# Optimization experiments

Measured on AMD Instinct MI355X. Metric: run time of the kernel, lower is better.

The kernel has to match this reference:

```python
import math
import jax, jax.numpy as jnp
import numpy as np

N, D, E, H = 4096, 512, 64, 8
LN_EPS = 1e-5


def setup_inputs() -> dict:
    key = jax.random.key(0)
    ks = jax.random.split(key, 6)
    return {
        "x": jax.random.normal(ks[0], (N, D), jnp.float32),
        "wq": jax.random.normal(ks[1], (H, D, E), jnp.float32) * 0.05,
        "wk": jax.random.normal(ks[2], (H, D, E), jnp.float32) * 0.05,
        "wv": jax.random.normal(ks[3], (H, D, E), jnp.float32) * 0.05,
        "w_mh": jax.random.normal(ks[4], (H * E, D), jnp.float32) * 0.05,
        "ln1_g": jnp.ones((D,), jnp.float32),
        "ln1_b": jnp.zeros((D,), jnp.float32),
        "ffn_w": jax.random.normal(ks[5], (D, D), jnp.float32) * 0.05,  # torch Linear weight [out,in]
        "ffn_b": jnp.zeros((D,), jnp.float32),
        "ln2_g": jnp.ones((D,), jnp.float32),
        "ln2_b": jnp.zeros((D,), jnp.float32),
    }


def _layernorm(y, g, b):
    m = y.mean(-1, keepdims=True)
    v = ((y - m) ** 2).mean(-1, keepdims=True)
    return (y - m) * jax.lax.rsqrt(v + LN_EPS) * g + b


def reference(x, wq, wk, wv, w_mh, ln1_g, ln1_b, ffn_w, ffn_b, ln2_g, ln2_b):
    dk = math.sqrt(wk.shape[-1])  # sqrt(embedding_size), as in the torch code
    q = jnp.einsum('nd,hde->hne', x, wq)  # [H,N,E]
    k = jnp.einsum('nd,hde->hne', x, wk)
    v = jnp.einsum('nd,hde->hne', x, wv)
    scores = jax.nn.softmax(jnp.einsum('hne,hme->hnm', q, k) / dk, axis=-1)  # [H,N,N]
    z = jnp.einsum('hnm,hme->hne', scores, v)  # [H,N,E]
    concat_z = jnp.transpose(z, (1, 0, 2)).reshape(x.shape[0], -1)  # [N, H*E]
    transformed_z = concat_z @ w_mh  # [N, D]
    normed_z = _layernorm(transformed_z + x, ln1_g, ln1_b)
    out = normed_z @ ffn_w.T + ffn_b  # nn.Linear
    return _layernorm(out + normed_z, ln2_g, ln2_b)
```

## Files before the change

kernel.cpp:

```cpp
#include <hip/hip_runtime.h>

#define NN 4096
#define DD 512
#define EE 64
#define HH 8

typedef _Float16 f16;
typedef f16 f16x4 __attribute__((ext_vector_type(4)));
typedef f16 f16x8 __attribute__((ext_vector_type(8)));
typedef float f32x4 __attribute__((ext_vector_type(4)));

__device__ __forceinline__ float hexp2(float x) { return __builtin_amdgcn_exp2f(x); }

__device__ void tile_transpose_cvt(const float* __restrict__ src, f16* __restrict__ dst,
                                   int R, int C, int bx, int by, int tid)
{
    __shared__ float t[32][33];
    const int tx = tid & 31, ty = tid >> 5;
    #pragma unroll
    for (int i = 0; i < 4; ++i) {
        int r = ty + i * 8;
        t[r][tx] = src[(size_t)(by + r) * C + bx + tx];
    }
    __syncthreads();
    #pragma unroll
    for (int i = 0; i < 4; ++i) {
        int c = ty + i * 8;
        dst[(size_t)(bx + c) * R + by + tx] = (f16)t[tx][c];
    }
}

__global__ __launch_bounds__(256) void prep_kernel(
    const float* __restrict__ x, const float* __restrict__ ffn_w,
    const float* __restrict__ wq, const float* __restrict__ wk, const float* __restrict__ wv,
    const float* __restrict__ w_mh,
    f16* __restrict__ xh, f16* __restrict__ ffnT, f16* __restrict__ wqkvT, f16* __restrict__ wmhT)
{
    const int job = blockIdx.y;
    const int tid = threadIdx.x;
    if (job == 0) {
        size_t i = ((size_t)blockIdx.x * 256 + tid) * 4;
        const size_t step = (size_t)256 * 256 * 4;
        for (; i < (size_t)NN * DD; i += step) {
            float4 t = *(const float4*)(x + i);
            f16x4 h = { (f16)t.x, (f16)t.y, (f16)t.z, (f16)t.w };
            *(f16x4*)(xh + i) = h;
        }
    } else if (job == 1) {
        size_t i = ((size_t)blockIdx.x * 256 + tid) * 4;
        float4 t = *(const float4*)(ffn_w + i);
        f16x4 h = { (f16)t.x, (f16)t.y, (f16)t.z, (f16)t.w };
        *(f16x4*)(ffnT + i) = h;
    } else if (job <= 4) {
        const float* src = (job == 2) ? wq : (job == 3) ? wk : wv;
        f16* dst = wqkvT + (size_t)(job - 2) * HH * EE * DD;
        const int z = blockIdx.x >> 5;
        const int tile = blockIdx.x & 31;
        tile_transpose_cvt(src + (size_t)z * DD * EE, dst + (size_t)z * DD * EE,
                           DD, EE, (tile & 1) * 32, (tile >> 1) * 32, tid);
    } else {
        const int tile = blockIdx.x;
        tile_transpose_cvt(w_mh, wmhT, DD, DD, (tile & 15) * 32, (tile >> 4) * 32, tid);
    }
}

__global__ __launch_bounds__(256) void qkv_mfma_kernel(
    const f16* __restrict__ A, const f16* __restrict__ BT,
    f16* __restrict__ qh, f16* __restrict__ kh, f16* __restrict__ vTh)
{
    __shared__ f16 As[64][72];
    __shared__ f16 Bs[64][72];
    const int tid = threadIdx.x;
    const int n0 = blockIdx.x * 64;
    const int cb = blockIdx.y;
    const int sel = cb >> 3, h = cb & 7;
    const f16* Arow = A + (size_t)n0 * DD;
    const f16* Brow = BT + (size_t)cb * 64 * DD;

    const int lane = tid & 63, wave = tid >> 6;
    const int l16 = lane & 15, quad = lane >> 4;
    const int m0 = wave * 16;

    const int r1 = tid >> 3, c1 = (tid & 7) * 8;
    const int r2 = (tid + 256) >> 3, c2 = ((tid + 256) & 7) * 8;

    f32x4 acc[4];
    #pragma unroll
    for (int t = 0; t < 4; ++t) acc[t] = (f32x4){0.f, 0.f, 0.f, 0.f};

    f16x8 a1 = *(const f16x8*)(Arow + (size_t)r1 * DD + c1);
    f16x8 a2 = *(const f16x8*)(Arow + (size_t)r2 * DD + c2);
    f16x8 b1 = *(const f16x8*)(Brow + (size_t)r1 * DD + c1);
    f16x8 b2 = *(const f16x8*)(Brow + (size_t)r2 * DD + c2);

    for (int kt = 0; kt < DD; kt += 64) {
        __syncthreads();
        *(f16x8*)(&As[r1][c1]) = a1;
        *(f16x8*)(&As[r2][c2]) = a2;
        *(f16x8*)(&Bs[r1][c1]) = b1;
        *(f16x8*)(&Bs[r2][c2]) = b2;
        __syncthreads();
        if (kt + 64 < DD) {
            a1 = *(const f16x8*)(Arow + (size_t)r1 * DD + kt + 64 + c1);
            a2 = *(const f16x8*)(Arow + (size_t)r2 * DD + kt + 64 + c2);
            b1 = *(const f16x8*)(Brow + (size_t)r1 * DD + kt + 64 + c1);
            b2 = *(const f16x8*)(Brow + (size_t)r2 * DD + kt + 64 + c2);
        }
        #pragma unroll
        for (int kk = 0; kk < 64; kk += 32) {
            f16x8 a = *(const f16x8*)(&As[m0 + l16][kk + quad * 8]);
            #pragma unroll
            for (int t = 0; t < 4; ++t) {
                f16x8 b = *(const f16x8*)(&Bs[t * 16 + l16][kk + quad * 8]);
                acc[t] = __builtin_amdgcn_mfma_f32_16x16x32_f16(a, b, acc[t], 0, 0, 0);
            }
        }
    }

    if (sel == 2) {
        #pragma unroll
        for (int t = 0; t < 4; ++t) {
            int e = t * 16 + l16;
            f16x4 v = { (f16)acc[t][0], (f16)acc[t][1], (f16)acc[t][2], (f16)acc[t][3] };
            *(f16x4*)(vTh + ((size_t)h * EE + e) * NN + n0 + m0 + quad * 4) = v;
        }
    } else {
        f16* o = (sel == 0) ? qh : kh;
        const float s = (sel == 0) ? 0.125f * 1.44269504088896f : 1.0f;
        #pragma unroll
        for (int r = 0; r < 4; ++r) {
            int row = n0 + m0 + quad * 4 + r;
            #pragma unroll
            for (int t = 0; t < 4; ++t)
                o[(size_t)h * NN * EE + (size_t)row * EE + t * 16 + l16] = (f16)(acc[t][r] * s);
        }
    }
}

#define BQ 128
#define BK 64
#define LK (BK + 12)

__global__ __launch_bounds__(256) void attn_mfma_kernel(
    const f16* __restrict__ q, const f16* __restrict__ k,
    const f16* __restrict__ vT, f16* __restrict__ Opart, float* __restrict__ lpart)
{
    __shared__ f16 Ks[BK][LK];
    __shared__ f16 VsT[EE][LK];

    const int tid = threadIdx.x;
    const int h = blockIdx.y;
    const int n0 = blockIdx.x * BQ;
    const int sp = blockIdx.z;
    const int nsp = gridDim.z;
    const int wave = tid >> 6;
    const int lane = tid & 63;
    const int l16 = lane & 15;
    const int quad = lane >> 4;
    const int m0 = wave * 16;

    const f16* qh = q + (size_t)h * NN * EE;
    const f16* kh = k + (size_t)h * NN * EE;
    const f16* vh = vT + (size_t)h * NN * EE;

    f16x8 qf[2][2];
    #pragma unroll
    for (int s = 0; s < 2; ++s) {
        const f16* qb = qh + (size_t)(n0 + s * 64 + m0 + l16) * EE;
        qf[s][0] = *(const f16x8*)(qb + quad * 8);
        qf[s][1] = *(const f16x8*)(qb + 32 + quad * 8);
    }

    float lp[2] = {0.f, 0.f};
    f32x4 O[2][4];
    #pragma unroll
    for (int s = 0; s < 2; ++s)
        #pragma unroll
        for (int t = 0; t < 4; ++t) O[s][t] = (f32x4){0.f, 0.f, 0.f, 0.f};

    const int span = NN / nsp;
    const int k_begin = sp * span;
    const int k_end = k_begin + span;

    const int srow = tid >> 3, sc8 = (tid & 7) * 8;
    const int srow2 = (tid + 256) >> 3, sc82 = ((tid + 256) & 7) * 8;
    #define KPERM(kk_) (((kk_) & 0x23) | (((kk_) & 0x04) << 2) | (((kk_) & 0x18) >> 1))
    const int prow1 = KPERM(srow), prow2 = KPERM(srow2);

    f16x8 kr0 = *(const f16x8*)(kh + (size_t)(k_begin + srow) * EE + sc8);
    f16x8 kr1 = *(const f16x8*)(kh + (size_t)(k_begin + srow2) * EE + sc82);
    f16x8 vr0 = *(const f16x8*)(vh + (size_t)srow * NN + k_begin + sc8);
    f16x8 vr1 = *(const f16x8*)(vh + (size_t)srow2 * NN + k_begin + sc82);

    for (int kt = k_begin; kt < k_end; kt += BK) {
        __syncthreads();
        *(f16x8*)(&Ks[prow1][sc8]) = kr0;
        *(f16x8*)(&Ks[prow2][sc82]) = kr1;
        *(f16x8*)(&VsT[srow][sc8]) = vr0;
        *(f16x8*)(&VsT[srow2][sc82]) = vr1;
        __syncthreads();

        if (kt + BK < k_end) {
            kr0 = *(const f16x8*)(kh + (size_t)(kt + BK + srow) * EE + sc8);
            kr1 = *(const f16x8*)(kh + (size_t)(kt + BK + srow2) * EE + sc82);
            vr0 = *(const f16x8*)(vh + (size_t)srow * NN + kt + BK + sc8);
            vr1 = *(const f16x8*)(vh + (size_t)srow2 * NN + kt + BK + sc82);
        }

        f16x8 bf[2][2];
        #pragma unroll
        for (int t = 0; t < 4; ++t) {
            f16x8 a0 = *(const f16x8*)(&Ks[t * 16 + l16][quad * 8]);
            f16x8 a1 = *(const f16x8*)(&Ks[t * 16 + l16][32 + quad * 8]);
            #pragma unroll
            for (int s = 0; s < 2; ++s) {
                f32x4 st = {0.f, 0.f, 0.f, 0.f};
                st = __builtin_amdgcn_mfma_f32_16x16x32_f16(a0, qf[s][0], st, 0, 0, 0);
                st = __builtin_amdgcn_mfma_f32_16x16x32_f16(a1, qf[s][1], st, 0, 0, 0);
                float p0 = hexp2(st[0]);
                float p1 = hexp2(st[1]);
                float p2 = hexp2(st[2]);
                float p3 = hexp2(st[3]);
                lp[s] += (p0 + p1) + (p2 + p3);
                f16x8& b = bf[s][t >> 1];
                const int o = (t & 1) * 4;
                b[o + 0] = (f16)p0; b[o + 1] = (f16)p1;
                b[o + 2] = (f16)p2; b[o + 3] = (f16)p3;
            }
        }

        #pragma unroll
        for (int te = 0; te < 4; ++te) {
            f16x8 v0 = *(const f16x8*)(&VsT[te * 16 + l16][quad * 8]);
            f16x8 v1 = *(const f16x8*)(&VsT[te * 16 + l16][32 + quad * 8]);
            #pragma unroll
            for (int s = 0; s < 2; ++s) {
                O[s][te] = __builtin_amdgcn_mfma_f32_16x16x32_f16(v0, bf[s][0], O[s][te], 0, 0, 0);
                O[s][te] = __builtin_amdgcn_mfma_f32_16x16x32_f16(v1, bf[s][1], O[s][te], 0, 0, 0);
            }
        }
    }

    #pragma unroll
    for (int s = 0; s < 2; ++s) {
        float l = lp[s];
        l += __shfl_xor(l, 16);
        l += __shfl_xor(l, 32);
        const int row = n0 + s * 64 + m0 + l16;
        if (quad == 0)
            lpart[(size_t)sp * HH * NN + (size_t)h * NN + row] = l;
        const float inv = 1.f / l;
        f16* obase = Opart + ((size_t)sp * NN + row) * DD + h * EE;
        #pragma unroll
        for (int te = 0; te < 4; ++te) {
            f16x4 v = { (f16)(O[s][te][0] * inv), (f16)(O[s][te][1] * inv),
                        (f16)(O[s][te][2] * inv), (f16)(O[s][te][3] * inv) };
            *(f16x4*)(obase + te * 16 + quad * 4) = v;
        }
    }
}

__global__ __launch_bounds__(256) void attn_combine_kernel(
    const f16* __restrict__ Opart, const float* __restrict__ lpart, f16* __restrict__ zh, int nsp)
{
    const size_t idx = ((size_t)blockIdx.x * 256 + threadIdx.x) * 8;
    const int n = (int)(idx >> 9);
    const int h = (int)((idx & 511) >> 6);
    float lw[8];
    float lsum = 0.f;
    for (int s = 0; s < nsp; ++s) {
        lw[s] = lpart[(size_t)s * HH * NN + (size_t)h * NN + n];
        lsum += lw[s];
    }
    const float inv = 1.f / lsum;
    float acc[8];
    #pragma unroll
    for (int i = 0; i < 8; ++i) acc[i] = 0.f;
    for (int s = 0; s < nsp; ++s) {
        f16x8 o = *(const f16x8*)(Opart + (size_t)s * NN * DD + idx);
        const float w = lw[s] * inv;
        #pragma unroll
        for (int i = 0; i < 8; ++i) acc[i] += w * (float)o[i];
    }
    f16x8 z;
    #pragma unroll
    for (int i = 0; i < 8; ++i) z[i] = (f16)acc[i];
    *(f16x8*)(zh + idx) = z;
}

__global__ __launch_bounds__(256) void gemm_mfma_kernel(
    const f16* __restrict__ A, const f16* __restrict__ BT,
    const float* __restrict__ bias, const float* __restrict__ resid32,
    const f16* __restrict__ resid16, float* __restrict__ out)
{
    __shared__ f16 As[64][72];
    __shared__ f16 Bs[64][72];
    const int tid = threadIdx.x;
    const int n0 = blockIdx.x * 64;
    const int j0 = blockIdx.y * 64;
    const f16* Arow = A + (size_t)n0 * DD;
    const f16* Brow = BT + (size_t)j0 * DD;

    const int lane = tid & 63, wave = tid >> 6;
    const int l16 = lane & 15, quad = lane >> 4;
    const int m0 = wave * 16;

    const int r1 = tid >> 3, c1 = (tid & 7) * 8;
    const int r2 = (tid + 256) >> 3, c2 = ((tid + 256) & 7) * 8;

    f32x4 acc[4];
    #pragma unroll
    for (int t = 0; t < 4; ++t) acc[t] = (f32x4){0.f, 0.f, 0.f, 0.f};

    f16x8 a1 = *(const f16x8*)(Arow + (size_t)r1 * DD + c1);
    f16x8 a2 = *(const f16x8*)(Arow + (size_t)r2 * DD + c2);
    f16x8 b1 = *(const f16x8*)(Brow + (size_t)r1 * DD + c1);
    f16x8 b2 = *(const f16x8*)(Brow + (size_t)r2 * DD + c2);

    for (int kt = 0; kt < DD; kt += 64) {
        __syncthreads();
        *(f16x8*)(&As[r1][c1]) = a1;
        *(f16x8*)(&As[r2][c2]) = a2;
        *(f16x8*)(&Bs[r1][c1]) = b1;
        *(f16x8*)(&Bs[r2][c2]) = b2;
        __syncthreads();
        if (kt + 64 < DD) {
            a1 = *(const f16x8*)(Arow + (size_t)r1 * DD + kt + 64 + c1);
            a2 = *(const f16x8*)(Arow + (size_t)r2 * DD + kt + 64 + c2);
            b1 = *(const f16x8*)(Brow + (size_t)r1 * DD + kt + 64 + c1);
            b2 = *(const f16x8*)(Brow + (size_t)r2 * DD + kt + 64 + c2);
        }
        #pragma unroll
        for (int kk = 0; kk < 64; kk += 32) {
            f16x8 a = *(const f16x8*)(&As[m0 + l16][kk + quad * 8]);
            #pragma unroll
            for (int t = 0; t < 4; ++t) {
                f16x8 b = *(const f16x8*)(&Bs[t * 16 + l16][kk + quad * 8]);
                acc[t] = __builtin_amdgcn_mfma_f32_16x16x32_f16(a, b, acc[t], 0, 0, 0);
            }
        }
    }

    #pragma unroll
    for (int r = 0; r < 4; ++r) {
        int row = n0 + m0 + quad * 4 + r;
        #pragma unroll
        for (int t = 0; t < 4; ++t) {
            int col = j0 + t * 16 + l16;
            float v = acc[t][r];
            if (bias)    v += bias[col];
            if (resid32) v += resid32[(size_t)row * DD + col];
            if (resid16) v += (float)resid16[(size_t)row * DD + col];
            out[(size_t)row * DD + col] = v;
        }
    }
}

__global__ __launch_bounds__(256) void ln_kernel(
    const float* __restrict__ y, const float* __restrict__ g, const float* __restrict__ b,
    f16* __restrict__ oh, float* __restrict__ of)
{
    const int lane = threadIdx.x & 63, wave = threadIdx.x >> 6;
    const int row = blockIdx.x * 4 + wave;
    const float* yr = y + (size_t)row * DD;
    f32x4 v0 = *(const f32x4*)(yr + lane * 4);
    f32x4 v1 = *(const f32x4*)(yr + 256 + lane * 4);
    float s = (v0[0] + v0[1]) + (v0[2] + v0[3]) + (v1[0] + v1[1]) + (v1[2] + v1[3]);
    float q = (v0[0]*v0[0] + v0[1]*v0[1]) + (v0[2]*v0[2] + v0[3]*v0[3])
            + (v1[0]*v1[0] + v1[1]*v1[1]) + (v1[2]*v1[2] + v1[3]*v1[3]);
    #pragma unroll
    for (int o = 1; o < 64; o <<= 1) { s += __shfl_xor(s, o); q += __shfl_xor(q, o); }
    float mean = s * (1.f / DD);
    float var = q * (1.f / DD) - mean * mean;
    float inv = rsqrtf(var + 1e-5f);

    f32x4 g0 = *(const f32x4*)(g + lane * 4);
    f32x4 g1 = *(const f32x4*)(g + 256 + lane * 4);
    f32x4 b0 = *(const f32x4*)(b + lane * 4);
    f32x4 b1 = *(const f32x4*)(b + 256 + lane * 4);
    f32x4 o0, o1;
    #pragma unroll
    for (int i = 0; i < 4; ++i) {
        o0[i] = (v0[i] - mean) * inv * g0[i] + b0[i];
        o1[i] = (v1[i] - mean) * inv * g1[i] + b1[i];
    }
    if (oh) {
        f16x4 h0 = { (f16)o0[0], (f16)o0[1], (f16)o0[2], (f16)o0[3] };
        f16x4 h1 = { (f16)o1[0], (f16)o1[1], (f16)o1[2], (f16)o1[3] };
        *(f16x4*)(oh + (size_t)row * DD + lane * 4) = h0;
        *(f16x4*)(oh + (size_t)row * DD + 256 + lane * 4) = h1;
    }
    if (of) {
        *(f32x4*)(of + (size_t)row * DD + lane * 4) = o0;
        *(f32x4*)(of + (size_t)row * DD + 256 + lane * 4) = o1;
    }
}

extern "C" void kernel_launch(void* const* d_in, const int* in_sizes, int n_in,
                              void* d_out, int out_size, void* d_ws, size_t ws_size,
                              hipStream_t stream) {
    const float* x     = (const float*)d_in[0];
    const float* wq    = (const float*)d_in[1];
    const float* wk    = (const float*)d_in[2];
    const float* wv    = (const float*)d_in[3];
    const float* w_mh  = (const float*)d_in[4];
    const float* ln1_g = (const float*)d_in[5];
    const float* ln1_b = (const float*)d_in[6];
    const float* ffn_w = (const float*)d_in[7];
    const float* ffn_b = (const float*)d_in[8];
    const float* ln2_g = (const float*)d_in[9];
    const float* ln2_b = (const float*)d_in[10];
    float* out = (float*)d_out;

    const size_t poolBytes = ((size_t)3 * HH * EE * DD + 2 * (size_t)DD * DD
                            + 3 * (size_t)HH * NN * EE + 2 * (size_t)NN * DD) * 2;
    int SP = 2;
    {
        size_t need8 = (size_t)8 * NN * DD * 2 + (size_t)8 * HH * NN * 4 + poolBytes + 4096;
        size_t need4 = (size_t)4 * NN * DD * 2 + (size_t)4 * HH * NN * 4 + poolBytes + 4096;
        if (ws_size >= need8) SP = 8; else if (ws_size >= need4) SP = 4;
    }

    char* base = (char*)d_ws;
    f16* Opart = (f16*)base;
    float* lpart = (float*)(base + (size_t)SP * NN * DD * 2);
    f16* xh   = (f16*)base;
    float* y  = (float*)base;
    size_t regionA = (size_t)SP * NN * DD * 2 + (size_t)SP * HH * NN * 4;
    regionA = (regionA + 255) & ~(size_t)255;
    f16* p = (f16*)(base + regionA);
    f16* wqkvT  = p; p += (size_t)3 * HH * EE * DD;
    f16* wmhT   = p; p += (size_t)DD * DD;
    f16* ffnT   = p; p += (size_t)DD * DD;
    f16* qh     = p; p += (size_t)HH * NN * EE;
    f16* kh     = p; p += (size_t)HH * NN * EE;
    f16* vTh    = p; p += (size_t)HH * NN * EE;
    f16* zh     = p; p += (size_t)NN * DD;
    f16* nzh    = p; p += (size_t)NN * DD;

    prep_kernel<<<dim3(256, 6), 256, 0, stream>>>(x, ffn_w, wq, wk, wv, w_mh,
                                                  xh, ffnT, wqkvT, wmhT);

    qkv_mfma_kernel<<<dim3(NN / 64, 24), 256, 0, stream>>>(xh, wqkvT, qh, kh, vTh);
    attn_mfma_kernel<<<dim3(NN / BQ, HH, SP), 256, 0, stream>>>(qh, kh, vTh, Opart, lpart);
    attn_combine_kernel<<<dim3(NN * DD / 2048), 256, 0, stream>>>(Opart, lpart, zh, SP);
    gemm_mfma_kernel<<<dim3(NN / 64, DD / 64), 256, 0, stream>>>(zh, wmhT, nullptr, x, nullptr, y);
    ln_kernel<<<dim3(NN / 4), 256, 0, stream>>>(y, ln1_g, ln1_b, nzh, nullptr);
    gemm_mfma_kernel<<<dim3(NN / 64, DD / 64), 256, 0, stream>>>(nzh, ffnT, ffn_b, nullptr, nzh, y);
    ln_kernel<<<dim3(NN / 4), 256, 0, stream>>>(y, ln2_g, ln2_b, nullptr, out);
}
```

Baseline: 188.7 us.

## Double-buffer LDS tiles, use fp16 intermediates, and cap attention split at four

```diff
diff --git a/kernel.cpp b/kernel.cpp
--- a/kernel.cpp
+++ b/kernel.cpp
@@ -68,8 +68,8 @@
     const f16* __restrict__ A, const f16* __restrict__ BT,
     f16* __restrict__ qh, f16* __restrict__ kh, f16* __restrict__ vTh)
 {
-    __shared__ f16 As[64][72];
-    __shared__ f16 Bs[64][72];
+    __shared__ f16 As[2][64][72];
+    __shared__ f16 Bs[2][64][72];
     const int tid = threadIdx.x;
     const int n0 = blockIdx.x * 64;
     const int cb = blockIdx.y;
@@ -93,12 +93,12 @@
     f16x8 b1 = *(const f16x8*)(Brow + (size_t)r1 * DD + c1);
     f16x8 b2 = *(const f16x8*)(Brow + (size_t)r2 * DD + c2);
 
+    int buf = 0;
     for (int kt = 0; kt < DD; kt += 64) {
-        __syncthreads();
-        *(f16x8*)(&As[r1][c1]) = a1;
-        *(f16x8*)(&As[r2][c2]) = a2;
-        *(f16x8*)(&Bs[r1][c1]) = b1;
-        *(f16x8*)(&Bs[r2][c2]) = b2;
+        *(f16x8*)(&As[buf][r1][c1]) = a1;
+        *(f16x8*)(&As[buf][r2][c2]) = a2;
+        *(f16x8*)(&Bs[buf][r1][c1]) = b1;
+        *(f16x8*)(&Bs[buf][r2][c2]) = b2;
         __syncthreads();
         if (kt + 64 < DD) {
             a1 = *(const f16x8*)(Arow + (size_t)r1 * DD + kt + 64 + c1);
@@ -108,13 +108,14 @@
         }
         #pragma unroll
         for (int kk = 0; kk < 64; kk += 32) {
-            f16x8 a = *(const f16x8*)(&As[m0 + l16][kk + quad * 8]);
+            f16x8 a = *(const f16x8*)(&As[buf][m0 + l16][kk + quad * 8]);
             #pragma unroll
             for (int t = 0; t < 4; ++t) {
-                f16x8 b = *(const f16x8*)(&Bs[t * 16 + l16][kk + quad * 8]);
+                f16x8 b = *(const f16x8*)(&Bs[buf][t * 16 + l16][kk + quad * 8]);
                 acc[t] = __builtin_amdgcn_mfma_f32_16x16x32_f16(a, b, acc[t], 0, 0, 0);
             }
         }
+        buf ^= 1;
     }
 
     if (sel == 2) {
@@ -145,8 +146,8 @@
     const f16* __restrict__ q, const f16* __restrict__ k,
     const f16* __restrict__ vT, f16* __restrict__ Opart, float* __restrict__ lpart)
 {
-    __shared__ f16 Ks[BK][LK];
-    __shared__ f16 VsT[EE][LK];
+    __shared__ f16 Ks[2][BK][LK];
+    __shared__ f16 VsT[2][EE][LK];
 
     const int tid = threadIdx.x;
     const int h = blockIdx.y;
@@ -192,12 +193,12 @@
     f16x8 vr0 = *(const f16x8*)(vh + (size_t)srow * NN + k_begin + sc8);
     f16x8 vr1 = *(const f16x8*)(vh + (size_t)srow2 * NN + k_begin + sc82);
 
+    int buf = 0;
     for (int kt = k_begin; kt < k_end; kt += BK) {
-        __syncthreads();
-        *(f16x8*)(&Ks[prow1][sc8]) = kr0;
-        *(f16x8*)(&Ks[prow2][sc82]) = kr1;
-        *(f16x8*)(&VsT[srow][sc8]) = vr0;
-        *(f16x8*)(&VsT[srow2][sc82]) = vr1;
+        *(f16x8*)(&Ks[buf][prow1][sc8]) = kr0;
+        *(f16x8*)(&Ks[buf][prow2][sc82]) = kr1;
+        *(f16x8*)(&VsT[buf][srow][sc8]) = vr0;
+        *(f16x8*)(&VsT[buf][srow2][sc82]) = vr1;
         __syncthreads();
 
         if (kt + BK < k_end) {
@@ -210,8 +211,8 @@
         f16x8 bf[2][2];
         #pragma unroll
         for (int t = 0; t < 4; ++t) {
-            f16x8 a0 = *(const f16x8*)(&Ks[t * 16 + l16][quad * 8]);
-            f16x8 a1 = *(const f16x8*)(&Ks[t * 16 + l16][32 + quad * 8]);
+            f16x8 a0 = *(const f16x8*)(&Ks[buf][t * 16 + l16][quad * 8]);
+            f16x8 a1 = *(const f16x8*)(&Ks[buf][t * 16 + l16][32 + quad * 8]);
             #pragma unroll
             for (int s = 0; s < 2; ++s) {
                 f32x4 st = {0.f, 0.f, 0.f, 0.f};
@@ -231,14 +232,15 @@
 
         #pragma unroll
         for (int te = 0; te < 4; ++te) {
-            f16x8 v0 = *(const f16x8*)(&VsT[te * 16 + l16][quad * 8]);
-            f16x8 v1 = *(const f16x8*)(&VsT[te * 16 + l16][32 + quad * 8]);
+            f16x8 v0 = *(const f16x8*)(&VsT[buf][te * 16 + l16][quad * 8]);
+            f16x8 v1 = *(const f16x8*)(&VsT[buf][te * 16 + l16][32 + quad * 8]);
             #pragma unroll
             for (int s = 0; s < 2; ++s) {
                 O[s][te] = __builtin_amdgcn_mfma_f32_16x16x32_f16(v0, bf[s][0], O[s][te], 0, 0, 0);
                 O[s][te] = __builtin_amdgcn_mfma_f32_16x16x32_f16(v1, bf[s][1], O[s][te], 0, 0, 0);
             }
         }
+        buf ^= 1;
     }
 
     #pragma unroll
@@ -290,11 +292,11 @@
 
 __global__ __launch_bounds__(256) void gemm_mfma_kernel(
     const f16* __restrict__ A, const f16* __restrict__ BT,
-    const float* __restrict__ bias, const float* __restrict__ resid32,
-    const f16* __restrict__ resid16, float* __restrict__ out)
-{
-    __shared__ f16 As[64][72];
-    __shared__ f16 Bs[64][72];
+    const float* __restrict__ bias, const f16* __restrict__ resid16,
+    f16* __restrict__ out)
+{
+    __shared__ f16 As[2][64][72];
+    __shared__ f16 Bs[2][64][72];
     const int tid = threadIdx.x;
     const int n0 = blockIdx.x * 64;
     const int j0 = blockIdx.y * 64;
@@ -317,12 +319,12 @@
     f16x8 b1 = *(const f16x8*)(Brow + (size_t)r1 * DD + c1);
     f16x8 b2 = *(const f16x8*)(Brow + (size_t)r2 * DD + c2);
 
+    int buf = 0;
     for (int kt = 0; kt < DD; kt += 64) {
-        __syncthreads();
-        *(f16x8*)(&As[r1][c1]) = a1;
-        *(f16x8*)(&As[r2][c2]) = a2;
-        *(f16x8*)(&Bs[r1][c1]) = b1;
-        *(f16x8*)(&Bs[r2][c2]) = b2;
+        *(f16x8*)(&As[buf][r1][c1]) = a1;
+        *(f16x8*)(&As[buf][r2][c2]) = a2;
+        *(f16x8*)(&Bs[buf][r1][c1]) = b1;
+        *(f16x8*)(&Bs[buf][r2][c2]) = b2;
         __syncthreads();
         if (kt + 64 < DD) {
             a1 = *(const f16x8*)(Arow + (size_t)r1 * DD + kt + 64 + c1);
@@ -332,13 +334,14 @@
         }
         #pragma unroll
         for (int kk = 0; kk < 64; kk += 32) {
-            f16x8 a = *(const f16x8*)(&As[m0 + l16][kk + quad * 8]);
+            f16x8 a = *(const f16x8*)(&As[buf][m0 + l16][kk + quad * 8]);
             #pragma unroll
             for (int t = 0; t < 4; ++t) {
-                f16x8 b = *(const f16x8*)(&Bs[t * 16 + l16][kk + quad * 8]);
+                f16x8 b = *(const f16x8*)(&Bs[buf][t * 16 + l16][kk + quad * 8]);
                 acc[t] = __builtin_amdgcn_mfma_f32_16x16x32_f16(a, b, acc[t], 0, 0, 0);
             }
         }
+        buf ^= 1;
     }
 
     #pragma unroll
@@ -349,50 +352,54 @@
             int col = j0 + t * 16 + l16;
             float v = acc[t][r];
             if (bias)    v += bias[col];
-            if (resid32) v += resid32[(size_t)row * DD + col];
             if (resid16) v += (float)resid16[(size_t)row * DD + col];
-            out[(size_t)row * DD + col] = v;
+            out[(size_t)row * DD + col] = (f16)v;
         }
     }
 }
 
 __global__ __launch_bounds__(256) void ln_kernel(
-    const float* __restrict__ y, const float* __restrict__ g, const float* __restrict__ b,
+    const f16* __restrict__ y, const float* __restrict__ g, const float* __restrict__ b,
     f16* __restrict__ oh, float* __restrict__ of)
 {
     const int lane = threadIdx.x & 63, wave = threadIdx.x >> 6;
     const int row = blockIdx.x * 4 + wave;
-    const float* yr = y + (size_t)row * DD;
-    f32x4 v0 = *(const f32x4*)(yr + lane * 4);
-    f32x4 v1 = *(const f32x4*)(yr + 256 + lane * 4);
-    float s = (v0[0] + v0[1]) + (v0[2] + v0[3]) + (v1[0] + v1[1]) + (v1[2] + v1[3]);
-    float q = (v0[0]*v0[0] + v0[1]*v0[1]) + (v0[2]*v0[2] + v0[3]*v0[3])
-            + (v1[0]*v1[0] + v1[1]*v1[1]) + (v1[2]*v1[2] + v1[3]*v1[3]);
+    f16x8 v = *(const f16x8*)(y + (size_t)row * DD + lane * 8);
+    float vf[8];
+    float s = 0.f, q = 0.f;
+    #pragma unroll
+    for (int i = 0; i < 8; ++i) {
+        vf[i] = (float)v[i];
+        s += vf[i];
+        q += vf[i] * vf[i];
+    }
     #pragma unroll
     for (int o = 1; o < 64; o <<= 1) { s += __shfl_xor(s, o); q += __shfl_xor(q, o); }
     float mean = s * (1.f / DD);
     float var = q * (1.f / DD) - mean * mean;
     float inv = rsqrtf(var + 1e-5f);
 
-    f32x4 g0 = *(const f32x4*)(g + lane * 4);
-    f32x4 g1 = *(const f32x4*)(g + 256 + lane * 4);
-    f32x4 b0 = *(const f32x4*)(b + lane * 4);
-    f32x4 b1 = *(const f32x4*)(b + 256 + lane * 4);
-    f32x4 o0, o1;
+    f32x4 g0 = *(const f32x4*)(g + lane * 8);
+    f32x4 g1 = *(const f32x4*)(g + lane * 8 + 4);
+    f32x4 b0 = *(const f32x4*)(b + lane * 8);
+    f32x4 b1 = *(const f32x4*)(b + lane * 8 + 4);
+    float o8[8];
     #pragma unroll
     for (int i = 0; i < 4; ++i) {
-        o0[i] = (v0[i] - mean) * inv * g0[i] + b0[i];
-        o1[i] = (v1[i] - mean) * inv * g1[i] + b1[i];
+        o8[i]     = (vf[i] - mean) * inv * g0[i] + b0[i];
+        o8[i + 4] = (vf[i + 4] - mean) * inv * g1[i] + b1[i];
     }
     if (oh) {
-        f16x4 h0 = { (f16)o0[0], (f16)o0[1], (f16)o0[2], (f16)o0[3] };
-        f16x4 h1 = { (f16)o1[0], (f16)o1[1], (f16)o1[2], (f16)o1[3] };
-        *(f16x4*)(oh + (size_t)row * DD + lane * 4) = h0;
-        *(f16x4*)(oh + (size_t)row * DD + 256 + lane * 4) = h1;
+        f16x8 hv;
+        #pragma unroll
+        for (int i = 0; i < 8; ++i) hv[i] = (f16)o8[i];
+        *(f16x8*)(oh + (size_t)row * DD + lane * 8) = hv;
     }
     if (of) {
-        *(f32x4*)(of + (size_t)row * DD + lane * 4) = o0;
-        *(f32x4*)(of + (size_t)row * DD + 256 + lane * 4) = o1;
+        f32x4 f0 = { o8[0], o8[1], o8[2], o8[3] };
+        f32x4 f1 = { o8[4], o8[5], o8[6], o8[7] };
+        *(f32x4*)(of + (size_t)row * DD + lane * 8) = f0;
+        *(f32x4*)(of + (size_t)row * DD + lane * 8 + 4) = f1;
     }
 }
 
@@ -413,19 +420,17 @@
     float* out = (float*)d_out;
 
     const size_t poolBytes = ((size_t)3 * HH * EE * DD + 2 * (size_t)DD * DD
-                            + 3 * (size_t)HH * NN * EE + 2 * (size_t)NN * DD) * 2;
+                            + 3 * (size_t)HH * NN * EE + 3 * (size_t)NN * DD) * 2;
     int SP = 2;
     {
-        size_t need8 = (size_t)8 * NN * DD * 2 + (size_t)8 * HH * NN * 4 + poolBytes + 4096;
         size_t need4 = (size_t)4 * NN * DD * 2 + (size_t)4 * HH * NN * 4 + poolBytes + 4096;
-        if (ws_size >= need8) SP = 8; else if (ws_size >= need4) SP = 4;
+        if (ws_size >= need4) SP = 4;
     }
 
     char* base = (char*)d_ws;
     f16* Opart = (f16*)base;
     float* lpart = (float*)(base + (size_t)SP * NN * DD * 2);
-    f16* xh   = (f16*)base;
-    float* y  = (float*)base;
+    f16* y16  = (f16*)base;
     size_t regionA = (size_t)SP * NN * DD * 2 + (size_t)SP * HH * NN * 4;
     regionA = (regionA + 255) & ~(size_t)255;
     f16* p = (f16*)(base + regionA);
@@ -437,6 +442,7 @@
     f16* vTh    = p; p += (size_t)HH * NN * EE;
     f16* zh     = p; p += (size_t)NN * DD;
     f16* nzh    = p; p += (size_t)NN * DD;
+    f16* xh     = p; p += (size_t)NN * DD;
 
     prep_kernel<<<dim3(256, 6), 256, 0, stream>>>(x, ffn_w, wq, wk, wv, w_mh,
                                                   xh, ffnT, wqkvT, wmhT);
@@ -444,8 +450,8 @@
     qkv_mfma_kernel<<<dim3(NN / 64, 24), 256, 0, stream>>>(xh, wqkvT, qh, kh, vTh);
     attn_mfma_kernel<<<dim3(NN / BQ, HH, SP), 256, 0, stream>>>(qh, kh, vTh, Opart, lpart);
     attn_combine_kernel<<<dim3(NN * DD / 2048), 256, 0, stream>>>(Opart, lpart, zh, SP);
-    gemm_mfma_kernel<<<dim3(NN / 64, DD / 64), 256, 0, stream>>>(zh, wmhT, nullptr, x, nullptr, y);
-    ln_kernel<<<dim3(NN / 4), 256, 0, stream>>>(y, ln1_g, ln1_b, nzh, nullptr);
-    gemm_mfma_kernel<<<dim3(NN / 64, DD / 64), 256, 0, stream>>>(nzh, ffnT, ffn_b, nullptr, nzh, y);
-    ln_kernel<<<dim3(NN / 4), 256, 0, stream>>>(y, ln2_g, ln2_b, nullptr, out);
-}
+    gemm_mfma_kernel<<<dim3(NN / 64, DD / 64), 256, 0, stream>>>(zh, wmhT, nullptr, xh, y16);
+    ln_kernel<<<dim3(NN / 4), 256, 0, stream>>>(y16, ln1_g, ln1_b, nzh, nullptr);
+    gemm_mfma_kernel<<<dim3(NN / 64, DD / 64), 256, 0, stream>>>(nzh, ffnT, ffn_b, nzh, y16);
+    ln_kernel<<<dim3(NN / 4), 256, 0, stream>>>(y16, ln2_g, ln2_b, nullptr, out);
+}
```

New measurement: 179.6 us. 4.8% less time.
